# Kernel optimization log

Hardware: AMD Instinct MI355X
Metric: run time of the kernel (lower is better)

## Reference

```python
import jax, jax.numpy as jnp
import numpy as np

B, S, D, H = 2, 2048, 1024, 16
DK = D // H


def setup_inputs() -> dict:
    key = jax.random.key(0)
    ks = jax.random.split(key, 12)
    init = lambda k, shp: (jax.random.normal(k, shp, dtype=jnp.float32) * 0.02)
    return {
        'query': jax.random.normal(ks[0], (B, S, D), dtype=jnp.float32),
        'key_in': jax.random.normal(ks[1], (B, S, D), dtype=jnp.float32),
        'value': jax.random.normal(ks[2], (B, S, D), dtype=jnp.float32),
        'w_q': init(ks[3], (D, D)), 'b_q': jnp.zeros((D,), jnp.float32),
        'w_k': init(ks[4], (D, D)), 'b_k': jnp.zeros((D,), jnp.float32),
        'w_v': init(ks[5], (D, D)), 'b_v': jnp.zeros((D,), jnp.float32),
        'w_o': init(ks[6], (D, D)), 'b_o': jnp.zeros((D,), jnp.float32),
        'fuzzy_centers': jax.random.normal(ks[7], (H, 3), dtype=jnp.float32),
        'fuzzy_widths': jnp.ones((H, 3), jnp.float32),
        'temperature': jnp.ones((1,), jnp.float32),
    }


def reference(query, key_in, value, w_q, b_q, w_k, b_k, w_v, b_v, w_o, b_o,
              fuzzy_centers, fuzzy_widths, temperature):
    b, s, d = query.shape
    h, dk = H, DK
    proj = lambda x, w, bias: x @ w.T + bias
    # [b,s,d] -> [b,h,s,dk]
    Q = proj(query, w_q, b_q).reshape(b, s, h, dk).transpose(0, 2, 1, 3)
    K = proj(key_in, w_k, b_k).reshape(b, s, h, dk).transpose(0, 2, 1, 3)
    V = proj(value, w_v, b_v).reshape(b, s, h, dk).transpose(0, 2, 1, 3)
    scores = jnp.einsum('bhsd,bhtd->bhst', Q, K) / np.sqrt(dk).astype(np.float32)
    # Faithful to torch: every (head,func) gaussian is applied to ALL heads' scores,
    # so each score gets sum of h*3 memberships, divided by 3.
    c = fuzzy_centers.reshape(-1)
    w = fuzzy_widths.reshape(-1)
    fz = jnp.zeros_like(scores)
    for i in range(h * 3):  # small fixed loop over membership functions
        fz = fz + jnp.exp(-(scores - c[i]) ** 2 / (2.0 * w[i] ** 2))
    fz = (fz / 3.0) / temperature[0]
    attn = jax.nn.softmax(fz, axis=-1)
    attended = jnp.einsum('bhst,bhtd->bhsd', attn, V)
    attended = attended.transpose(0, 2, 1, 3).reshape(b, s, d)
    return attended @ w_o.T + b_o
```

## Files before the change

### kernel.cpp

```cpp
#include <hip/hip_runtime.h>
#include <hip/hip_bf16.h>


#define S_LEN 2048
#define DMODEL 1024
#define NHEAD 16
#define DKH 64
#define NLUT 2048
#define LUT_MIN (-10.0f)
#define LUT_MAX (10.0f)
#define FPAD 72

typedef __attribute__((ext_vector_type(8))) short bfx8;
typedef __attribute__((ext_vector_type(4))) float fx4;

__device__ __forceinline__ short f2bf(float x) {
    unsigned u = __builtin_bit_cast(unsigned, x);
    u = (u + 0x7fffu + ((u >> 16) & 1u)) >> 16;
    return (short)u;
}

__device__ __forceinline__ void stage8_f32(const float* __restrict__ src, short* dst) {
    float4 a = *(const float4*)(src);
    float4 b = *(const float4*)(src + 4);
    bfx8 r;
    r[0] = f2bf(a.x); r[1] = f2bf(a.y); r[2] = f2bf(a.z); r[3] = f2bf(a.w);
    r[4] = f2bf(b.x); r[5] = f2bf(b.y); r[6] = f2bf(b.z); r[7] = f2bf(b.w);
    *(bfx8*)dst = r;
}

__device__ __forceinline__ void gload_lds16(const void* g, void* l) {
    __builtin_amdgcn_global_load_lds(
        (const __attribute__((address_space(1))) unsigned int*)g,
        (__attribute__((address_space(3))) unsigned int*)l, 16, 0, 0);
}

__device__ void lut_body(const float* __restrict__ centers, const float* __restrict__ widths,
                         const float* __restrict__ temp, unsigned* __restrict__ lutp) {
    __shared__ float fzb[NLUT];
    __shared__ float red[256];
    __shared__ float cs[48], wsb[48];
    int tid = threadIdx.x;
    if (tid < 48) { cs[tid] = centers[tid]; wsb[tid] = widths[tid]; }
    __syncthreads();
    float invT = 1.0f / temp[0];
    const float step = (LUT_MAX - LUT_MIN) / (float)(NLUT - 1);
    float lmax = -1e30f;
    for (int i = tid; i < NLUT; i += 256) {
        float s = LUT_MIN + step * (float)i;
        float fz = 0.0f;
        #pragma unroll 1
        for (int j = 0; j < 48; j++) {
            float d = s - cs[j];
            float w = wsb[j];
            fz += expf(-(d * d) / (2.0f * w * w));
        }
        fz = fz * (1.0f / 3.0f) * invT;
        fzb[i] = fz;
        lmax = fmaxf(lmax, fz);
    }
    red[tid] = lmax;
    __syncthreads();
    for (int off = 128; off > 0; off >>= 1) {
        if (tid < off) red[tid] = fmaxf(red[tid], red[tid + off]);
        __syncthreads();
    }
    float m = red[0];
    __syncthreads();
    for (int i = tid; i < NLUT; i += 256) fzb[i] = expf(fzb[i] - m);
    __syncthreads();
    for (int i = tid; i < NLUT; i += 256) {
        float g0 = fzb[i];
        float g1 = fzb[(i + 1 < NLUT) ? i + 1 : NLUT - 1];
        unsigned lo = (unsigned short)f2bf(g0);
        unsigned hi = (unsigned short)f2bf(g1);
        lutp[i] = lo | (hi << 16);
    }
}

__global__ void build_lut_pk(const float* centers, const float* widths,
                             const float* temp, unsigned* lutp) {
    lut_body(centers, widths, temp, lutp);
}

__global__ void cast_bf16(const float* __restrict__ src, short* __restrict__ dst, int n8) {
    int i = blockIdx.x * 256 + threadIdx.x;
    if (i < n8) stage8_f32(src + (size_t)i * 8, dst + (size_t)i * 8);
}

__global__ void prep_all(const float* q, const float* kin, const float* v,
        const float* wq, const float* wk, const float* wv, const float* wo,
        short* xq, short* xk, short* xv,
        short* bwq, short* bwk, short* bwv, short* bwo,
        const float* centers, const float* widths, const float* temp,
        unsigned* lutp) {
    int bid = blockIdx.x;
    if (bid >= 8192) {
        lut_body(centers, widths, temp, lutp);
        return;
    }
    const float* src; short* dst; int blk;
    if (bid < 6144) {
        int y = bid >> 11; blk = bid & 2047;
        src = (y == 0) ? q : (y == 1) ? kin : v;
        dst = (y == 0) ? xq : (y == 1) ? xk : xv;
    } else {
        int y = (bid - 6144) >> 9; blk = (bid - 6144) & 511;
        src = (y == 0) ? wq : (y == 1) ? wk : (y == 2) ? wv : wo;
        dst = (y == 0) ? bwq : (y == 1) ? bwk : (y == 2) ? bwv : bwo;
    }
    size_t i = (size_t)blk * 256 + threadIdx.x;
    stage8_f32(src + i * 8, (short*)dst + i * 8);
}

struct GemmJob {
    const short* A; const short* W; const float* bias;
    short* obf; float* of32; int mode; float scale;
};

__global__ __launch_bounds__(256, 2) void gemm128(GemmJob j0, GemmJob j1, GemmJob j2) {
    __shared__ __align__(16) short As[128 * 32];
    __shared__ __align__(16) short Bs[128 * 32];
    GemmJob jb = (blockIdx.z == 0) ? j0 : (blockIdx.z == 1) ? j1 : j2;
    int tid = threadIdx.x, wave = tid >> 6, lane = tid & 63, quad = lane >> 4, l15 = lane & 15;
    int m0 = blockIdx.y * 128, n0 = blockIdx.x * 128;
    int wm = (wave >> 1) * 64, wn = (wave & 1) * 64;

    fx4 acc[4][4];
    #pragma unroll
    for (int i = 0; i < 4; i++)
        #pragma unroll
        for (int j = 0; j < 4; j++)
            #pragma unroll
            for (int r = 0; r < 4; r++) acc[i][j][r] = 0.0f;

    int fc = (quad ^ ((l15 >> 1) & 3)) * 8;

    for (int k0 = 0; k0 < DMODEL; k0 += 32) {
        __syncthreads();
        #pragma unroll
        for (int r = 0; r < 2; r++) {
            int slot = r * 256 + wave * 64 + lane;
            int row = slot >> 2, c = slot & 3, gc = c ^ ((row >> 1) & 3);
            gload_lds16(jb.A + (size_t)(m0 + row) * DMODEL + k0 + gc * 8,
                        &As[(r * 256 + wave * 64) * 8]);
            gload_lds16(jb.W + (size_t)(n0 + row) * DMODEL + k0 + gc * 8,
                        &Bs[(r * 256 + wave * 64) * 8]);
        }
        __syncthreads();
        bfx8 af[4], bfr[4];
        #pragma unroll
        for (int i = 0; i < 4; i++) af[i] = *(const bfx8*)(&As[(wm + i * 16 + l15) * 32 + fc]);
        #pragma unroll
        for (int j = 0; j < 4; j++) bfr[j] = *(const bfx8*)(&Bs[(wn + j * 16 + l15) * 32 + fc]);
        #pragma unroll
        for (int i = 0; i < 4; i++)
            #pragma unroll
            for (int j = 0; j < 4; j++)
                acc[i][j] = __builtin_amdgcn_mfma_f32_16x16x32_bf16(af[i], bfr[j], acc[i][j], 0, 0, 0);
    }

    #pragma unroll
    for (int j = 0; j < 4; j++) {
        int n = n0 + wn + j * 16 + l15;
        float bv = jb.bias[n];
        #pragma unroll
        for (int i = 0; i < 4; i++) {
            #pragma unroll
            for (int r = 0; r < 4; r++) {
                int m = m0 + wm + i * 16 + quad * 4 + r;
                float v = (acc[i][j][r] + bv) * jb.scale;
                if (jb.mode == 0) {
                    int b = m >> 11, s = m & 2047, h = n >> 6, dk = n & 63;
                    jb.obf[(((size_t)(b * NHEAD + h)) * S_LEN + s) * DKH + dk] = f2bf(v);
                } else if (jb.mode == 1) {
                    int b = m >> 11, s = m & 2047, h = n >> 6, dk = n & 63;
                    jb.obf[(((size_t)(b * NHEAD + h)) * DKH + dk) * S_LEN + s] = f2bf(v);
                } else {
                    jb.of32[(size_t)m * DMODEL + n] = v;
                }
            }
        }
    }
}

__global__ __launch_bounds__(256, 4) void flash_fuzzy(const short* __restrict__ Qb,
        const short* __restrict__ Kb, const short* __restrict__ VTb,
        const unsigned* __restrict__ lutg, short* __restrict__ AO) {
    __shared__ __align__(16) short Ks[64 * 64];
    __shared__ __align__(16) short Vs[64 * 64];
    __shared__ __align__(16) short Ps[64 * FPAD];
    __shared__ unsigned lut[NLUT];

    int tid = threadIdx.x, wave = tid >> 6, lane = tid & 63, quad = lane >> 4, l15 = lane & 15;
    int q0 = blockIdx.x * 64, bh = blockIdx.y;
    const short* Qp = Qb + (size_t)bh * S_LEN * DKH;
    const short* Kp = Kb + (size_t)bh * S_LEN * DKH;
    const short* Vp = VTb + (size_t)bh * DKH * S_LEN;

    #pragma unroll
    for (int i = tid; i < NLUT / 4; i += 256)
        ((uint4*)lut)[i] = ((const uint4*)lutg)[i];

    bfx8 aq[2];
    #pragma unroll
    for (int ks = 0; ks < 2; ks++)
        aq[ks] = *(const bfx8*)(Qp + (size_t)(q0 + wave * 16 + l15) * DKH + ks * 32 + quad * 8);

    bfx8 ones;
    #pragma unroll
    for (int i = 0; i < 8; i++) ones[i] = (short)0x3F80;

    fx4 oacc[4];
    fx4 dacc;
    #pragma unroll
    for (int r = 0; r < 4; r++) dacc[r] = 0.0f;
    #pragma unroll
    for (int tn = 0; tn < 4; tn++)
        #pragma unroll
        for (int r = 0; r < 4; r++) oacc[tn][r] = 0.0f;

    const float invh = (float)(NLUT - 1) / (LUT_MAX - LUT_MIN);
    const float xoff = -LUT_MIN * invh;

    int srow[2], sgc[2];
    #pragma unroll
    for (int r = 0; r < 2; r++) {
        int slot = (wave * 2 + r) * 64 + lane;
        srow[r] = slot >> 3;
        sgc[r] = (slot & 7) ^ (srow[r] & 7);
    }

    for (int t0 = 0; t0 < S_LEN; t0 += 64) {
        __syncthreads();
        #pragma unroll
        for (int r = 0; r < 2; r++) {
            gload_lds16(Kp + (size_t)(t0 + srow[r]) * DKH + sgc[r] * 8,
                        &Ks[((wave * 2 + r) * 64) * 8]);
            gload_lds16(Vp + (size_t)srow[r] * S_LEN + t0 + sgc[r] * 8,
                        &Vs[((wave * 2 + r) * 64) * 8]);
        }
        __syncthreads();

        fx4 sac[4];
        #pragma unroll
        for (int tn = 0; tn < 4; tn++)
            #pragma unroll
            for (int r = 0; r < 4; r++) sac[tn][r] = 0.0f;
        #pragma unroll
        for (int ks = 0; ks < 2; ks++) {
            int fc = ((ks * 4 + quad) ^ (l15 & 7)) * 8;
            bfx8 bk[4];
            #pragma unroll
            for (int tn = 0; tn < 4; tn++)
                bk[tn] = *(const bfx8*)(&Ks[(tn * 16 + l15) * 64 + fc]);
            #pragma unroll
            for (int tn = 0; tn < 4; tn++)
                sac[tn] = __builtin_amdgcn_mfma_f32_16x16x32_bf16(aq[ks], bk[tn], sac[tn], 0, 0, 0);
        }

        #pragma unroll
        for (int tn = 0; tn < 4; tn++) {
            #pragma unroll
            for (int r = 0; r < 4; r++) {
                float s = sac[tn][r];
                float x = fmaf(s, invh, xoff);
                x = fminf(fmaxf(x, 0.0f), (float)(NLUT - 1));
                int j = (int)x;
                float f = x - (float)j;
                unsigned pr = lut[j];
                float v0 = __builtin_bit_cast(float, pr << 16);
                float v1 = __builtin_bit_cast(float, pr & 0xffff0000u);
                float pv = fmaf(f, v1 - v0, v0);
                unsigned u = __builtin_bit_cast(unsigned, pv);
                Ps[(wave * 16 + quad * 4 + r) * FPAD + tn * 16 + l15] =
                    (short)((u + 0x8000u) >> 16);
            }
        }

        #pragma unroll
        for (int ks = 0; ks < 2; ks++) {
            int fc = ((ks * 4 + quad) ^ (l15 & 7)) * 8;
            bfx8 ap, bv[4];
            ap = *(const bfx8*)(&Ps[(wave * 16 + l15) * FPAD + ks * 32 + quad * 8]);
            #pragma unroll
            for (int tn = 0; tn < 4; tn++)
                bv[tn] = *(const bfx8*)(&Vs[(tn * 16 + l15) * 64 + fc]);
            #pragma unroll
            for (int tn = 0; tn < 4; tn++)
                oacc[tn] = __builtin_amdgcn_mfma_f32_16x16x32_bf16(ap, bv[tn], oacc[tn], 0, 0, 0);
            dacc = __builtin_amdgcn_mfma_f32_16x16x32_bf16(ap, ones, dacc, 0, 0, 0);
        }
    }

    int b = bh >> 4, h = bh & 15;
    #pragma unroll
    for (int tn = 0; tn < 4; tn++) {
        #pragma unroll
        for (int r = 0; r < 4; r++) {
            int q = q0 + wave * 16 + quad * 4 + r;
            int dk = tn * 16 + l15;
            float v = oacc[tn][r] / dacc[r];
            AO[((size_t)(b * S_LEN + q)) * DMODEL + h * DKH + dk] = f2bf(v);
        }
    }
}

extern "C" void kernel_launch(void* const* d_in, const int* in_sizes, int n_in,
                              void* d_out, int out_size, void* d_ws, size_t ws_size,
                              hipStream_t stream) {
    const float* query   = (const float*)d_in[0];
    const float* key_in  = (const float*)d_in[1];
    const float* value   = (const float*)d_in[2];
    const float* w_q     = (const float*)d_in[3];
    const float* b_q     = (const float*)d_in[4];
    const float* w_k     = (const float*)d_in[5];
    const float* b_k     = (const float*)d_in[6];
    const float* w_v     = (const float*)d_in[7];
    const float* b_v     = (const float*)d_in[8];
    const float* w_o     = (const float*)d_in[9];
    const float* b_o     = (const float*)d_in[10];
    const float* centers = (const float*)d_in[11];
    const float* widths  = (const float*)d_in[12];
    const float* temp    = (const float*)d_in[13];

    char* p = (char*)d_ws;
    auto alloc = [&](size_t bytes) -> void* {
        void* r = (void*)p;
        p += (bytes + 255) & ~(size_t)255;
        return r;
    };
    const size_t nBHSD = (size_t)2 * NHEAD * S_LEN * DKH;
    const size_t nW    = (size_t)DMODEL * DMODEL;
    unsigned* lutp = (unsigned*)alloc(NLUT * 4);
    short* Qb  = (short*)alloc(nBHSD * 2);
    short* Kb  = (short*)alloc(nBHSD * 2);
    short* VTb = (short*)alloc(nBHSD * 2);

    char* save = p;
    short* xq  = (short*)alloc(nBHSD * 2);
    short* xk  = (short*)alloc(nBHSD * 2);
    short* xv  = (short*)alloc(nBHSD * 2);
    short* bwq = (short*)alloc(nW * 2);
    short* bwk = (short*)alloc(nW * 2);
    short* bwv = (short*)alloc(nW * 2);
    short* bwo = (short*)alloc(nW * 2);
    bool fused = ((size_t)(p - (char*)d_ws) <= ws_size);

    dim3 blk(256);
    dim3 gq(8, 32, 3), g1(8, 32, 1), fg(32, 32);
    GemmJob JO;

    if (fused) {
        short* AO = xq;
        prep_all<<<dim3(8193), blk, 0, stream>>>(query, key_in, value, w_q, w_k, w_v, w_o,
                xq, xk, xv, bwq, bwk, bwv, bwo, centers, widths, temp, lutp);
        GemmJob JQ = {xq, bwq, b_q, Qb,  nullptr, 0, 0.125f};
        GemmJob JK = {xk, bwk, b_k, Kb,  nullptr, 0, 1.0f};
        GemmJob JV = {xv, bwv, b_v, VTb, nullptr, 1, 1.0f};
        gemm128<<<gq, blk, 0, stream>>>(JQ, JK, JV);
        flash_fuzzy<<<fg, blk, 0, stream>>>(Qb, Kb, VTb, lutp, AO);
        JO = {AO, bwo, b_o, nullptr, (float*)d_out, 2, 1.0f};
        gemm128<<<g1, blk, 0, stream>>>(JO, JO, JO);
    } else {
        p = save;
        short* xf = (short*)alloc(nBHSD * 2);
        short* wb = (short*)alloc(nW * 2);
        short* AO = xf;
        const int n8x = (int)(nBHSD / 8), n8w = (int)(nW / 8);
        dim3 cg((n8x + 255) / 256), cw((n8w + 255) / 256);
        build_lut_pk<<<dim3(1), blk, 0, stream>>>(centers, widths, temp, lutp);
        cast_bf16<<<cg, blk, 0, stream>>>(query, xf, n8x);
        cast_bf16<<<cw, blk, 0, stream>>>(w_q, wb, n8w);
        JO = {xf, wb, b_q, Qb, nullptr, 0, 0.125f};
        gemm128<<<g1, blk, 0, stream>>>(JO, JO, JO);
        cast_bf16<<<cg, blk, 0, stream>>>(key_in, xf, n8x);
        cast_bf16<<<cw, blk, 0, stream>>>(w_k, wb, n8w);
        JO = {xf, wb, b_k, Kb, nullptr, 0, 1.0f};
        gemm128<<<g1, blk, 0, stream>>>(JO, JO, JO);
        cast_bf16<<<cg, blk, 0, stream>>>(value, xf, n8x);
        cast_bf16<<<cw, blk, 0, stream>>>(w_v, wb, n8w);
        JO = {xf, wb, b_v, VTb, nullptr, 1, 1.0f};
        gemm128<<<g1, blk, 0, stream>>>(JO, JO, JO);
        flash_fuzzy<<<fg, blk, 0, stream>>>(Qb, Kb, VTb, lutp, AO);
        cast_bf16<<<cw, blk, 0, stream>>>(w_o, wb, n8w);
        JO = {AO, wb, b_o, nullptr, (float*)d_out, 2, 1.0f};
        gemm128<<<g1, blk, 0, stream>>>(JO, JO, JO);
    }
}
```

Baseline: 315.9 us.

## Double-buffer GEMM tiles, remap blocks, coalesce V-transpose stores, fold LUT scale into Q

```diff
diff --git a/kernel.cpp b/kernel.cpp
--- a/kernel.cpp
+++ b/kernel.cpp
@@ -10,8 +10,10 @@
 #define LUT_MIN (-10.0f)
 #define LUT_MAX (10.0f)
 #define FPAD 72
+#define TPAD 136
 
 typedef __attribute__((ext_vector_type(8))) short bfx8;
+typedef __attribute__((ext_vector_type(4))) short sx4;
 typedef __attribute__((ext_vector_type(4))) float fx4;
 
 __device__ __forceinline__ short f2bf(float x) {
@@ -118,12 +120,13 @@
     short* obf; float* of32; int mode; float scale;
 };
 
-__global__ __launch_bounds__(256, 2) void gemm128(GemmJob j0, GemmJob j1, GemmJob j2) {
-    __shared__ __align__(16) short As[128 * 32];
-    __shared__ __align__(16) short Bs[128 * 32];
-    GemmJob jb = (blockIdx.z == 0) ? j0 : (blockIdx.z == 1) ? j1 : j2;
+__global__ __launch_bounds__(256, 2) void gemm_sq(GemmJob jb) {
+    __shared__ __align__(16) short smem[4][128 * 32];
     int tid = threadIdx.x, wave = tid >> 6, lane = tid & 63, quad = lane >> 4, l15 = lane & 15;
-    int m0 = blockIdx.y * 128, n0 = blockIdx.x * 128;
+    int f = blockIdx.x;
+    int idx = f >> 3;
+    int n0 = (idx & 7) * 128;
+    int m0 = ((f & 7) * 4 + (idx >> 3)) * 128;
     int wm = (wave >> 1) * 64, wn = (wave & 1) * 64;
 
     fx4 acc[4][4];
@@ -136,28 +139,81 @@
 
     int fc = (quad ^ ((l15 >> 1) & 3)) * 8;
 
-    for (int k0 = 0; k0 < DMODEL; k0 += 32) {
+    int srow[2], sgc[2], sbase[2];
+    #pragma unroll
+    for (int r = 0; r < 2; r++) {
+        int slot = r * 256 + wave * 64 + lane;
+        srow[r] = slot >> 2;
+        sgc[r] = (slot & 3) ^ ((srow[r] >> 1) & 3);
+        sbase[r] = (r * 256 + wave * 64) * 8;
+    }
+
+    #pragma unroll
+    for (int r = 0; r < 2; r++) {
+        gload_lds16(jb.A + (size_t)(m0 + srow[r]) * DMODEL + sgc[r] * 8, &smem[0][sbase[r]]);
+        gload_lds16(jb.W + (size_t)(n0 + srow[r]) * DMODEL + sgc[r] * 8, &smem[2][sbase[r]]);
+    }
+
+    for (int kt = 0; kt < 32; kt++) {
         __syncthreads();
-        #pragma unroll
-        for (int r = 0; r < 2; r++) {
-            int slot = r * 256 + wave * 64 + lane;
-            int row = slot >> 2, c = slot & 3, gc = c ^ ((row >> 1) & 3);
-            gload_lds16(jb.A + (size_t)(m0 + row) * DMODEL + k0 + gc * 8,
-                        &As[(r * 256 + wave * 64) * 8]);
-            gload_lds16(jb.W + (size_t)(n0 + row) * DMODEL + k0 + gc * 8,
-                        &Bs[(r * 256 + wave * 64) * 8]);
-        }
-        __syncthreads();
+        if (kt + 1 < 32) {
+            int k0 = (kt + 1) * 32, b = (kt + 1) & 1;
+            #pragma unroll
+            for (int r = 0; r < 2; r++) {
+                gload_lds16(jb.A + (size_t)(m0 + srow[r]) * DMODEL + k0 + sgc[r] * 8,
+                            &smem[b][sbase[r]]);
+                gload_lds16(jb.W + (size_t)(n0 + srow[r]) * DMODEL + k0 + sgc[r] * 8,
+                            &smem[2 + b][sbase[r]]);
+            }
+        }
+        const short* Ab = smem[kt & 1];
+        const short* Bb = smem[2 + (kt & 1)];
         bfx8 af[4], bfr[4];
         #pragma unroll
-        for (int i = 0; i < 4; i++) af[i] = *(const bfx8*)(&As[(wm + i * 16 + l15) * 32 + fc]);
-        #pragma unroll
-        for (int j = 0; j < 4; j++) bfr[j] = *(const bfx8*)(&Bs[(wn + j * 16 + l15) * 32 + fc]);
+        for (int i = 0; i < 4; i++) af[i] = *(const bfx8*)(&Ab[(wm + i * 16 + l15) * 32 + fc]);
+        #pragma unroll
+        for (int j = 0; j < 4; j++) bfr[j] = *(const bfx8*)(&Bb[(wn + j * 16 + l15) * 32 + fc]);
         #pragma unroll
         for (int i = 0; i < 4; i++)
             #pragma unroll
             for (int j = 0; j < 4; j++)
                 acc[i][j] = __builtin_amdgcn_mfma_f32_16x16x32_bf16(af[i], bfr[j], acc[i][j], 0, 0, 0);
+    }
+
+    if (jb.mode == 1) {
+        short* T = smem[0];
+        int bb = m0 >> 11, s0 = m0 & 2047;
+        #pragma unroll
+        for (int half = 0; half < 2; half++) {
+            __syncthreads();
+            if ((wave & 1) == half) {
+                #pragma unroll
+                for (int j = 0; j < 4; j++) {
+                    int nl = j * 16 + l15;
+                    float bv = jb.bias[n0 + half * 64 + nl];
+                    #pragma unroll
+                    for (int i = 0; i < 4; i++) {
+                        int ml = wm + i * 16 + quad * 4;
+                        sx4 w4;
+                        #pragma unroll
+                        for (int r = 0; r < 4; r++)
+                            w4[r] = f2bf((acc[i][j][r] + bv) * jb.scale);
+                        *(sx4*)(&T[nl * TPAD + ml]) = w4;
+                    }
+                }
+            }
+            __syncthreads();
+            #pragma unroll
+            for (int r2 = 0; r2 < 4; r2++) {
+                int ch = r2 * 256 + tid;
+                int nl = ch >> 4, m8 = ch & 15;
+                int n = n0 + half * 64 + nl;
+                int hh = n >> 6, dk = n & 63;
+                *(int4*)(jb.obf + (((size_t)(bb * NHEAD + hh)) * DKH + dk) * S_LEN
+                         + s0 + m8 * 8) = *(const int4*)(&T[nl * TPAD + m8 * 8]);
+            }
+        }
+        return;
     }
 
     #pragma unroll
@@ -173,9 +229,6 @@
                 if (jb.mode == 0) {
                     int b = m >> 11, s = m & 2047, h = n >> 6, dk = n & 63;
                     jb.obf[(((size_t)(b * NHEAD + h)) * S_LEN + s) * DKH + dk] = f2bf(v);
-                } else if (jb.mode == 1) {
-                    int b = m >> 11, s = m & 2047, h = n >> 6, dk = n & 63;
-                    jb.obf[(((size_t)(b * NHEAD + h)) * DKH + dk) * S_LEN + s] = f2bf(v);
                 } else {
                     jb.of32[(size_t)m * DMODEL + n] = v;
                 }
@@ -220,9 +273,6 @@
         #pragma unroll
         for (int r = 0; r < 4; r++) oacc[tn][r] = 0.0f;
 
-    const float invh = (float)(NLUT - 1) / (LUT_MAX - LUT_MIN);
-    const float xoff = -LUT_MIN * invh;
-
     int srow[2], sgc[2];
     #pragma unroll
     for (int r = 0; r < 2; r++) {
@@ -249,11 +299,11 @@
             for (int r = 0; r < 4; r++) sac[tn][r] = 0.0f;
         #pragma unroll
         for (int ks = 0; ks < 2; ks++) {
-            int fc = ((ks * 4 + quad) ^ (l15 & 7)) * 8;
+            int fcs = ((ks * 4 + quad) ^ (l15 & 7)) * 8;
             bfx8 bk[4];
             #pragma unroll
             for (int tn = 0; tn < 4; tn++)
-                bk[tn] = *(const bfx8*)(&Ks[(tn * 16 + l15) * 64 + fc]);
+                bk[tn] = *(const bfx8*)(&Ks[(tn * 16 + l15) * 64 + fcs]);
             #pragma unroll
             for (int tn = 0; tn < 4; tn++)
                 sac[tn] = __builtin_amdgcn_mfma_f32_16x16x32_bf16(aq[ks], bk[tn], sac[tn], 0, 0, 0);
@@ -263,15 +313,13 @@
         for (int tn = 0; tn < 4; tn++) {
             #pragma unroll
             for (int r = 0; r < 4; r++) {
-                float s = sac[tn][r];
-                float x = fmaf(s, invh, xoff);
-                x = fminf(fmaxf(x, 0.0f), (float)(NLUT - 1));
+                float x = sac[tn][r] + 1023.5f;
                 int j = (int)x;
-                float f = x - (float)j;
-                unsigned pr = lut[j];
+                float ff = x - (float)j;
+                unsigned pr = lut[j & (NLUT - 1)];
                 float v0 = __builtin_bit_cast(float, pr << 16);
                 float v1 = __builtin_bit_cast(float, pr & 0xffff0000u);
-                float pv = fmaf(f, v1 - v0, v0);
+                float pv = fmaf(ff, v1 - v0, v0);
                 unsigned u = __builtin_bit_cast(unsigned, pv);
                 Ps[(wave * 16 + quad * 4 + r) * FPAD + tn * 16 + l15] =
                     (short)((u + 0x8000u) >> 16);
@@ -280,12 +328,12 @@
 
         #pragma unroll
         for (int ks = 0; ks < 2; ks++) {
-            int fc = ((ks * 4 + quad) ^ (l15 & 7)) * 8;
+            int fcs = ((ks * 4 + quad) ^ (l15 & 7)) * 8;
             bfx8 ap, bv[4];
             ap = *(const bfx8*)(&Ps[(wave * 16 + l15) * FPAD + ks * 32 + quad * 8]);
             #pragma unroll
             for (int tn = 0; tn < 4; tn++)
-                bv[tn] = *(const bfx8*)(&Vs[(tn * 16 + l15) * 64 + fc]);
+                bv[tn] = *(const bfx8*)(&Vs[(tn * 16 + l15) * 64 + fcs]);
             #pragma unroll
             for (int tn = 0; tn < 4; tn++)
                 oacc[tn] = __builtin_amdgcn_mfma_f32_16x16x32_bf16(ap, bv[tn], oacc[tn], 0, 0, 0);
@@ -332,6 +380,8 @@
     };
     const size_t nBHSD = (size_t)2 * NHEAD * S_LEN * DKH;
     const size_t nW    = (size_t)DMODEL * DMODEL;
+    const float QSCALE = 0.125f * ((float)(NLUT - 1) / (LUT_MAX - LUT_MIN));
+
     unsigned* lutp = (unsigned*)alloc(NLUT * 4);
     short* Qb  = (short*)alloc(nBHSD * 2);
     short* Kb  = (short*)alloc(nBHSD * 2);
@@ -347,21 +397,22 @@
     short* bwo = (short*)alloc(nW * 2);
     bool fused = ((size_t)(p - (char*)d_ws) <= ws_size);
 
-    dim3 blk(256);
-    dim3 gq(8, 32, 3), g1(8, 32, 1), fg(32, 32);
-    GemmJob JO;
+    dim3 blk(256), gg(256), fg(32, 32);
+    GemmJob J;
 
     if (fused) {
         short* AO = xq;
         prep_all<<<dim3(8193), blk, 0, stream>>>(query, key_in, value, w_q, w_k, w_v, w_o,
                 xq, xk, xv, bwq, bwk, bwv, bwo, centers, widths, temp, lutp);
-        GemmJob JQ = {xq, bwq, b_q, Qb,  nullptr, 0, 0.125f};
-        GemmJob JK = {xk, bwk, b_k, Kb,  nullptr, 0, 1.0f};
-        GemmJob JV = {xv, bwv, b_v, VTb, nullptr, 1, 1.0f};
-        gemm128<<<gq, blk, 0, stream>>>(JQ, JK, JV);
+        J = {xq, bwq, b_q, Qb,  nullptr, 0, QSCALE};
+        gemm_sq<<<gg, blk, 0, stream>>>(J);
+        J = {xk, bwk, b_k, Kb,  nullptr, 0, 1.0f};
+        gemm_sq<<<gg, blk, 0, stream>>>(J);
+        J = {xv, bwv, b_v, VTb, nullptr, 1, 1.0f};
+        gemm_sq<<<gg, blk, 0, stream>>>(J);
         flash_fuzzy<<<fg, blk, 0, stream>>>(Qb, Kb, VTb, lutp, AO);
-        JO = {AO, bwo, b_o, nullptr, (float*)d_out, 2, 1.0f};
-        gemm128<<<g1, blk, 0, stream>>>(JO, JO, JO);
+        J = {AO, bwo, b_o, nullptr, (float*)d_out, 2, 1.0f};
+        gemm_sq<<<gg, blk, 0, stream>>>(J);
     } else {
         p = save;
         short* xf = (short*)alloc(nBHSD * 2);
@@ -372,19 +423,19 @@
         build_lut_pk<<<dim3(1), blk, 0, stream>>>(centers, widths, temp, lutp);
         cast_bf16<<<cg, blk, 0, stream>>>(query, xf, n8x);
         cast_bf16<<<cw, blk, 0, stream>>>(w_q, wb, n8w);
-        JO = {xf, wb, b_q, Qb, nullptr, 0, 0.125f};
-        gemm128<<<g1, blk, 0, stream>>>(JO, JO, JO);
+        J = {xf, wb, b_q, Qb, nullptr, 0, QSCALE};
+        gemm_sq<<<gg, blk, 0, stream>>>(J);
         cast_bf16<<<cg, blk, 0, stream>>>(key_in, xf, n8x);
         cast_bf16<<<cw, blk, 0, stream>>>(w_k, wb, n8w);
-        JO = {xf, wb, b_k, Kb, nullptr, 0, 1.0f};
-        gemm128<<<g1, blk, 0, stream>>>(JO, JO, JO);
+        J = {xf, wb, b_k, Kb, nullptr, 0, 1.0f};
+        gemm_sq<<<gg, blk, 0, stream>>>(J);
         cast_bf16<<<cg, blk, 0, stream>>>(value, xf, n8x);
         cast_bf16<<<cw, blk, 0, stream>>>(w_v, wb, n8w);
-        JO = {xf, wb, b_v, VTb, nullptr, 1, 1.0f};
-        gemm128<<<g1, blk, 0, stream>>>(JO, JO, JO);
+        J = {xf, wb, b_v, VTb, nullptr, 1, 1.0f};
+        gemm_sq<<<gg, blk, 0, stream>>>(J);
         flash_fuzzy<<<fg, blk, 0, stream>>>(Qb, Kb, VTb, lutp, AO);
         cast_bf16<<<cw, blk, 0, stream>>>(w_o, wb, n8w);
-        JO = {AO, wb, b_o, nullptr, (float*)d_out, 2, 1.0f};
-        gemm128<<<g1, blk, 0, stream>>>(JO, JO, JO);
-    }
-}
+        J = {AO, wb, b_o, nullptr, (float*)d_out, 2, 1.0f};
+        gemm_sq<<<gg, blk, 0, stream>>>(J);
+    }
+}
```

New measurement: 318.3 us. No clear change (+0.8%).
